# Kernel optimization log

Measured on AMD Instinct MI355X. Metric: run time of the kernel, lower is better.

## Reference

```python
import jax, jax.numpy as jnp
import numpy as np

NE, NU, E = 200000, 100000, 1000000
F_IN, H, OUT = 64, 128, 2
GRID_SIZE, K = 5, 3  # efficient-kan defaults: grid_size=5, spline_order=3
NB = GRID_SIZE + K    # number of b-spline bases per input feature = 8


def make_grid(in_features):
    h = 2.0 / GRID_SIZE  # grid_range [-1, 1]
    g = jnp.arange(-K, GRID_SIZE + K + 1, dtype=jnp.float32) * h - 1.0  # [GRID_SIZE+2K+1]
    return jnp.tile(g[None, :], (in_features, 1))  # [in, 12]


def b_splines(x, grid):
    # x: [N, in], grid: [in, G]; Cox-de Boor recursion -> [N, in, G-K-1]
    x = x[..., None]
    bases = ((x >= grid[:, :-1]) & (x < grid[:, 1:])).astype(x.dtype)
    for j in range(1, K + 1):
        bases = ((x - grid[:, :-(j + 1)]) / (grid[:, j:-1] - grid[:, :-(j + 1)])) * bases[..., :-1] \
              + ((grid[:, j + 1:] - x) / (grid[:, j + 1:] - grid[:, 1:-j])) * bases[..., 1:]
    return bases


def kan_linear(x, base_w, spline_w, scaler, grid):
    base = jax.nn.silu(x) @ base_w.T                       # [N, out]
    sw = spline_w * scaler[..., None]                      # [out, in, NB]
    spline = jnp.einsum('nik,oik->no', b_splines(x, grid), sw)
    return base + spline


def sage_conv(x_src, x_dst, ei, w_n, b_n, w_r):
    # PyG SAGEConv: lin_l(mean_j x_j) + lin_r(x_i); bias only on lin_l
    src, dst = ei[0], ei[1]
    msg = jnp.take(x_src, src, axis=0)                                  # [E, H] gather
    s = jax.ops.segment_sum(msg, dst, num_segments=x_dst.shape[0])      # scatter-sum
    cnt = jax.ops.segment_sum(jnp.ones(src.shape, x_src.dtype), dst, num_segments=x_dst.shape[0])
    mean = s / jnp.maximum(cnt, 1.0)[:, None]
    return mean @ w_n.T + b_n + x_dst @ w_r.T


def setup_inputs():
    key = jax.random.key(0)
    ks = jax.random.split(key, 40)
    inp = {}
    inp['x_email'] = jax.random.normal(ks[0], (NE, F_IN), jnp.float32)
    inp['ei_ue'] = jnp.stack([jax.random.randint(ks[1], (E,), 0, NU),
                              jax.random.randint(ks[2], (E,), 0, NE)])
    inp['ei_eu'] = jnp.stack([jax.random.randint(ks[3], (E,), 0, NE),
                              jax.random.randint(ks[4], (E,), 0, NU)])
    inp['w_email'] = jax.random.normal(ks[5], (H, F_IN), jnp.float32) * 0.05
    inp['b_email'] = jnp.zeros((H,), jnp.float32)
    inp['emb_user'] = jax.random.normal(ks[6], (NU, H), jnp.float32) * 0.05
    i = 7
    for name in ['l1_ue', 'l1_eu', 'l2_ue', 'l2_eu']:
        inp['w_' + name + '_n'] = jax.random.normal(ks[i], (H, H), jnp.float32) * 0.05; i += 1
        inp['b_' + name] = jnp.zeros((H,), jnp.float32)
        inp['w_' + name + '_r'] = jax.random.normal(ks[i], (H, H), jnp.float32) * 0.05; i += 1
    inp['kan1_base'] = jax.random.normal(ks[i], (64, H), jnp.float32) * 0.05; i += 1
    inp['kan1_spline'] = jax.random.normal(ks[i], (64, H, NB), jnp.float32) * 0.05; i += 1
    inp['kan1_scaler'] = 1.0 + jax.random.normal(ks[i], (64, H), jnp.float32) * 0.05; i += 1
    inp['grid1'] = make_grid(H)
    inp['kan2_base'] = jax.random.normal(ks[i], (OUT, 64), jnp.float32) * 0.05; i += 1
    inp['kan2_spline'] = jax.random.normal(ks[i], (OUT, 64, NB), jnp.float32) * 0.05; i += 1
    inp['kan2_scaler'] = 1.0 + jax.random.normal(ks[i], (OUT, 64), jnp.float32) * 0.05; i += 1
    inp['grid2'] = make_grid(64)
    return inp


def reference(x_email, ei_ue, ei_eu, w_email, b_email, emb_user,
              w_l1_ue_n, b_l1_ue, w_l1_ue_r, w_l1_eu_n, b_l1_eu, w_l1_eu_r,
              w_l2_ue_n, b_l2_ue, w_l2_ue_r, w_l2_eu_n, b_l2_eu, w_l2_eu_r,
              kan1_base, kan1_spline, kan1_scaler, grid1,
              kan2_base, kan2_spline, kan2_scaler, grid2):
    xe = x_email @ w_email.T + b_email      # email_lin
    xu = emb_user                            # embedding(arange(NU)) == full table
    # hetero SAGE layer 1 (to_hetero aggr='sum'; one inbound edge type per dst)
    e1 = jax.nn.relu(sage_conv(xu, xe, ei_ue, w_l1_ue_n, b_l1_ue, w_l1_ue_r))
    u1 = jax.nn.relu(sage_conv(xe, xu, ei_eu, w_l1_eu_n, b_l1_eu, w_l1_eu_r))
    # dropout(p=0.5) is identity in eval mode
    # layer 2: only the email output feeds the KAN head (user-dst conv2 output is unused)
    e2 = jax.nn.relu(sage_conv(u1, e1, ei_ue, w_l2_ue_n, b_l2_ue, w_l2_ue_r))
    h = kan_linear(e2, kan1_base, kan1_spline, kan1_scaler, grid1)
    out = kan_linear(h, kan2_base, kan2_spline, kan2_scaler, grid2)
    return out
```

## Files before the change

### kernel.cpp

```cpp
#include <hip/hip_runtime.h>
#include <hip/hip_bf16.h>

typedef __attribute__((ext_vector_type(8))) short short8;
typedef __attribute__((ext_vector_type(4))) float f32x4;

static constexpr int kNE  = 200000;
static constexpr int kNU  = 100000;
static constexpr int kE   = 1000000;
static constexpr int kGrpU = kNE / 8;
static constexpr int kGrpE = kNU / 8;

static constexpr long long SZ_NEH = (long long)kNE * 128;
static constexpr long long SZ_NUH = (long long)kNU * 128;
static constexpr long long O_B0   = 64;
static constexpr long long O_B1   = O_B0 + SZ_NEH;
static constexpr long long O_B2   = O_B1 + SZ_NEH;
static constexpr long long O_W    = O_B2 + SZ_NUH;
static constexpr long long O_BEM  = O_W;
static constexpr long long O_BL1  = O_BEM + 128;
static constexpr long long O_BEN  = O_BL1 + 128;
static constexpr long long O_BL2  = O_BEN + 128;
static constexpr long long O_GRID1= O_BL2 + 128;
static constexpr long long O_BASE2= O_GRID1 + 1536;
static constexpr long long O_GRID2= O_BASE2 + 128;
static constexpr long long O_SW2  = O_GRID2 + 768;
static constexpr long long I_CNT_UE = O_SW2 + 1024;
static constexpr long long I_CNT_EU = I_CNT_UE + kNE;
static constexpr long long I_RO_UE  = I_CNT_EU + kNU;
static constexpr long long I_RO_EU  = I_RO_UE + kNE;
static constexpr long long I_CUR_UE = I_RO_EU + kNU;
static constexpr long long I_CUR_EU = I_CUR_UE + kNE;
static constexpr long long I_SRT_UE = I_CUR_EU + kNU;
static constexpr long long I_SRT_EU = I_SRT_UE + kE;
static constexpr long long I_BSUM_UE= I_SRT_EU + kE;
static constexpr long long I_BOFF_UE= I_BSUM_UE + 256;
static constexpr long long I_BSUM_EU= I_BOFF_UE + 256;
static constexpr long long I_BOFF_EU= I_BSUM_EU + 256;
static constexpr long long FR_BASE_I= (I_BOFF_EU + 256 + 7) & ~7LL;
static constexpr long long U_WEM   = 0;
static constexpr long long U_W1N   = U_WEM + 8192;
static constexpr long long U_W1R   = U_W1N + 16384;
static constexpr long long U_WEN   = U_W1R + 16384;
static constexpr long long U_WER   = U_WEN + 16384;
static constexpr long long U_W2N   = U_WER + 16384;
static constexpr long long U_W2R   = U_W2N + 16384;
static constexpr long long U_BASE1 = U_W2R + 16384;
static constexpr long long U_SW1H  = U_BASE1 + 8192;
static constexpr long long U_SW1L  = U_SW1H + 65536;

__device__ __forceinline__ float bf2f(unsigned short u) {
    return __uint_as_float(((unsigned)u) << 16);
}
__device__ __forceinline__ unsigned short f2bf_rne(float f) {
    unsigned u = __float_as_uint(f);
    return (unsigned short)((u + 0x7fffu + ((u >> 16) & 1u)) >> 16);
}
__device__ __forceinline__ void split2(float x, unsigned short& hi, unsigned short& lo) {
    hi = f2bf_rne(x);
    lo = f2bf_rne(x - bf2f(hi));
}
__device__ __forceinline__ float btrunc(float x) {
    return __uint_as_float(__float_as_uint(x) & 0xffff0000u);
}
__device__ __forceinline__ unsigned pack_hi2(float x0, float x1) {
    return __builtin_amdgcn_perm(__float_as_uint(x1), __float_as_uint(x0), 0x07060302u);
}
__device__ __forceinline__ void split8_trunc(const float* __restrict__ xv, short8& ah, short8& al) {
    unsigned* hp = (unsigned*)&ah;
    unsigned* lp = (unsigned*)&al;
#pragma unroll
    for (int jp = 0; jp < 4; jp++) {
        const float x0 = xv[2 * jp], x1 = xv[2 * jp + 1];
        const float l0 = x0 - btrunc(x0), l1 = x1 - btrunc(x1);
        hp[jp] = pack_hi2(x0, x1);
        lp[jp] = pack_hi2(l0, l1);
    }
}
__device__ __forceinline__ int get_isbf(const unsigned* __restrict__ g) {
    return (g[0] == 0xC00CCCCDu) ? 0 : 1;
}

__device__ __forceinline__ void pack128_one(const void* __restrict__ src, unsigned short* __restrict__ dst,
                                            int K, int t, int isbf) {
    const int lane = t & 63;
    const int nt = (t >> 6) % 8;
    const int kt = (t >> 6) / 8;
    const int n = nt * 16 + (lane & 15);
    const int k0 = kt * 32 + (lane >> 4) * 8;
    unsigned short* d = dst + (((size_t)(kt * 8 + nt) * 64 + lane) << 3);
#pragma unroll
    for (int j = 0; j < 8; j++) {
        float f = isbf ? bf2f(((const unsigned short*)src)[(size_t)n * K + k0 + j])
                       : ((const float*)src)[(size_t)n * K + k0 + j];
        d[j] = f2bf_rne(f);
    }
}

__device__ __forceinline__ void base1_one(const void* __restrict__ src, unsigned short* __restrict__ dst,
                                          int t, int isbf) {
    const int lane = t & 63, nt = (t >> 6) & 3, kt = t >> 8;
    const int n = nt * 16 + (lane & 15);
    const int k0 = kt * 32 + (lane >> 4) * 8;
    unsigned short* d = dst + (((size_t)(kt * 4 + nt) * 64 + lane) << 3);
#pragma unroll
    for (int j = 0; j < 8; j++) {
        float f = isbf ? bf2f(((const unsigned short*)src)[n * 128 + k0 + j])
                       : ((const float*)src)[n * 128 + k0 + j];
        d[j] = f2bf_rne(f);
    }
}

__device__ __forceinline__ void sw1_one(const void* __restrict__ sp, const void* __restrict__ sc,
                                        unsigned short* __restrict__ dh, unsigned short* __restrict__ dl,
                                        int t, int isbf) {
    const int lane = t & 63, nt = (t >> 6) & 3, kt = t >> 8;
    const int n = nt * 16 + (lane & 15);
    const int k0 = kt * 32 + (lane >> 4) * 8;
    const float scal = isbf ? bf2f(((const unsigned short*)sc)[n * 128 + (k0 >> 3)])
                            : ((const float*)sc)[n * 128 + (k0 >> 3)];
    const size_t base = ((size_t)(kt * 4 + nt) * 64 + lane) << 3;
#pragma unroll
    for (int j = 0; j < 8; j++) {
        float f = isbf ? bf2f(((const unsigned short*)sp)[(size_t)n * 1024 + k0 + j])
                       : ((const float*)sp)[(size_t)n * 1024 + k0 + j];
        float p = f * scal;
        unsigned short hi, lo;
        split2(p, hi, lo);
        dh[base + j] = hi;
        dl[base + j] = lo;
    }
}

struct PrepArgs {
    const void* csrc[7];  int coff[7];  int cn[7];
    const void* psrc[7];  unsigned pdst[7];  int pK[7];
    const void* sp2;  const void* sc2;
    const void* b1src;  const void* swsp;  const void* swsc;
};

__global__ __launch_bounds__(256) void prep_kernel(PrepArgs A, float* __restrict__ wsf,
                                                   int* __restrict__ wsi,
                                                   unsigned short* __restrict__ fbase,
                                                   const unsigned* __restrict__ gdet) {
    const int isbf = get_isbf(gdet);
    const int t0 = blockIdx.x * 256 + threadIdx.x;
    const int gs = gridDim.x * 256;
    for (int i = t0; i < kNE + kNU; i += gs) wsi[I_CNT_UE + i] = 0;
    for (int t = 0; t < 7; t++) {
        const int n = A.cn[t];
        const void* s = A.csrc[t];
        float* d = wsf + A.coff[t];
        for (int i = t0; i < n; i += gs)
            d[i] = isbf ? bf2f(((const unsigned short*)s)[i]) : ((const float*)s)[i];
    }
    for (int i = t0; i < 1024; i += gs) {
        float a = isbf ? bf2f(((const unsigned short*)A.sp2)[i]) : ((const float*)A.sp2)[i];
        float b = isbf ? bf2f(((const unsigned short*)A.sc2)[i >> 3]) : ((const float*)A.sc2)[i >> 3];
        wsf[O_SW2 + i] = a * b;
    }
    for (int t = 0; t < 7; t++) {
        const int K = A.pK[t];
        const int tot = (K / 32) * 8 * 64;
        unsigned short* dst = fbase + A.pdst[t];
        const void* src = A.psrc[t];
        for (int i = t0; i < tot; i += gs) pack128_one(src, dst, K, i, isbf);
    }
    for (int i = t0; i < 1024; i += gs) base1_one(A.b1src, fbase + U_BASE1, i, isbf);
    for (int i = t0; i < 8192; i += gs)
        sw1_one(A.swsp, A.swsc, fbase + U_SW1H, fbase + U_SW1L, i, isbf);
}

__global__ __launch_bounds__(256) void hist_both(const int* __restrict__ ue, const int* __restrict__ eu,
                                                 int* __restrict__ cntU, int* __restrict__ cntE) {
    const int g = blockIdx.x & 7;
    const int loU = g * kGrpU, hiU = loU + kGrpU;
    const int loE = g * kGrpE, hiE = loE + kGrpE;
    const int stride = (gridDim.x >> 3) * 256;
    for (int i = (blockIdx.x >> 3) * 256 + threadIdx.x; i < kE; i += stride) {
        const int d = ue[kE + i];
        if (d >= loU && d < hiU) atomicAdd(&cntU[d], 1);
        const int d2 = eu[kE + i];
        if (d2 >= loE && d2 < hiE) atomicAdd(&cntE[d2], 1);
    }
}

__global__ __launch_bounds__(256) void scan1_both(const int* __restrict__ cntU, int* __restrict__ roU,
                                                  int* __restrict__ bsU, const int* __restrict__ cntE,
                                                  int* __restrict__ roE, int* __restrict__ bsE) {
    __shared__ int sc[256];
    int b = blockIdx.x;
    const int* cnt;  int* ro;  int* bsum;  int n;
    if (b < 196) { cnt = cntU; ro = roU; bsum = bsU; n = kNE; }
    else { b -= 196; cnt = cntE; ro = roE; bsum = bsE; n = kNU; }
    const int t = threadIdx.x;
    const int i0 = b * 1024 + t * 4;
    int c[4];
#pragma unroll
    for (int q = 0; q < 4; q++) c[q] = (i0 + q < n) ? cnt[i0 + q] : 0;
    int s = c[0] + c[1] + c[2] + c[3];
    sc[t] = s;
    __syncthreads();
    for (int off = 1; off < 256; off <<= 1) {
        int v = (t >= off) ? sc[t - off] : 0;
        __syncthreads();
        sc[t] += v;
        __syncthreads();
    }
    int run = sc[t] - s;
#pragma unroll
    for (int q = 0; q < 4; q++) {
        if (i0 + q < n) ro[i0 + q] = run;
        run += c[q];
    }
    if (t == 255) bsum[b] = sc[255];
}

__global__ __launch_bounds__(256) void scan2_both(const int* __restrict__ bsU, int* __restrict__ boU,
                                                  const int* __restrict__ bsE, int* __restrict__ boE) {
    __shared__ int sc[256];
    const int* bsum;  int* boff;  int nb;
    if (blockIdx.x == 0) { bsum = bsU; boff = boU; nb = 196; }
    else { bsum = bsE; boff = boE; nb = 98; }
    const int t = threadIdx.x;
    int s = (t < nb) ? bsum[t] : 0;
    sc[t] = s;
    __syncthreads();
    for (int off = 1; off < 256; off <<= 1) {
        int v = (t >= off) ? sc[t - off] : 0;
        __syncthreads();
        sc[t] += v;
        __syncthreads();
    }
    if (t < nb) boff[t] = sc[t] - s;
}

__global__ __launch_bounds__(256) void scan3_both(int* __restrict__ roU, int* __restrict__ curU,
                                                  const int* __restrict__ boU, int* __restrict__ roE,
                                                  int* __restrict__ curE, const int* __restrict__ boE) {
    const int stride = gridDim.x * blockDim.x;
    for (int i = blockIdx.x * blockDim.x + threadIdx.x; i < kNE + kNU; i += stride) {
        if (i < kNE) {
            int v = roU[i] + boU[i >> 10];
            roU[i] = v;
            curU[i] = v;
        } else {
            int j = i - kNE;
            int v = roE[j] + boE[j >> 10];
            roE[j] = v;
            curE[j] = v;
        }
    }
}

__global__ __launch_bounds__(256) void fill_both(const int* __restrict__ ue, const int* __restrict__ eu,
                                                 int* __restrict__ curU, int* __restrict__ srtU,
                                                 int* __restrict__ curE, int* __restrict__ srtE) {
    const int g = blockIdx.x & 7;
    const int loU = g * kGrpU, hiU = loU + kGrpU;
    const int loE = g * kGrpE, hiE = loE + kGrpE;
    const int stride = (gridDim.x >> 3) * 256;
    for (int i = (blockIdx.x >> 3) * 256 + threadIdx.x; i < kE; i += stride) {
        const int d = ue[kE + i];
        if (d >= loU && d < hiU) {
            const int pos = atomicAdd(&curU[d], 1);
            srtU[pos] = ue[i];
        }
        const int d2 = eu[kE + i];
        if (d2 >= loE && d2 < hiE) {
            const int pos = atomicAdd(&curE[d2], 1);
            srtE[pos] = eu[i];
        }
    }
}

template <int KD, bool RAW, int THREADS>
__device__ __forceinline__ void stage_tile(float (*Xs)[132], const void* __restrict__ Av, int r0, int N,
                                           int tid, int isbf) {
    constexpr int TPR = THREADS / 64;
    constexpr int per = KD / TPR;
    const int row = tid / TPR;
    const int cq = (tid % TPR) * per;
    const size_t gr = (size_t)min(r0 + row, N - 1);
    if (RAW && isbf) {
        const unsigned short* p = (const unsigned short*)Av + gr * KD + cq;
#pragma unroll
        for (int v = 0; v < per; v += 8) {
            short8 s = *(const short8*)(p + v);
#pragma unroll
            for (int j = 0; j < 8; j++) Xs[row][cq + v + j] = bf2f(((unsigned short*)&s)[j]);
        }
    } else {
        const float* p = (const float*)Av + gr * KD + cq;
#pragma unroll
        for (int v = 0; v < per; v += 4) *(float4*)&Xs[row][cq + v] = *(const float4*)(p + v);
    }
}

template <int KT, int NT>
__device__ __forceinline__ void gemm_phase(float (*Xs)[132], const unsigned short* __restrict__ Wf,
                                           f32x4* acc, int rowl, int q, int lane, int ntBase) {
#pragma unroll
    for (int kt = 0; kt < KT; kt++) {
        float xv[8];
        *(float4*)&xv[0] = *(const float4*)&Xs[rowl][kt * 32 + q * 8];
        *(float4*)&xv[4] = *(const float4*)&Xs[rowl][kt * 32 + q * 8 + 4];
        short8 ah, al;
        split8_trunc(xv, ah, al);
#pragma unroll
        for (int nt = 0; nt < NT; nt++) {
            short8 b = *(const short8*)(Wf + (((size_t)(kt * 8 + ntBase + nt) * 64 + lane) << 3));
            acc[nt] = __builtin_amdgcn_mfma_f32_16x16x32_bf16(ah, b, acc[nt], 0, 0, 0);
            acc[nt] = __builtin_amdgcn_mfma_f32_16x16x32_bf16(al, b, acc[nt], 0, 0, 0);
        }
    }
}

__global__ __launch_bounds__(256) void lin_xe(const void* __restrict__ A1,
                                              const unsigned short* __restrict__ W1f,
                                              const float* __restrict__ bias, float* __restrict__ out, int N,
                                              const unsigned* __restrict__ gdet) {
    __shared__ float Xs[64][132];
    const int tid = threadIdx.x;
    const int wave = tid >> 6, lane = tid & 63;
    const int m = lane & 15, q = lane >> 4;
    const int r0 = blockIdx.x * 64;
    const int isbf = get_isbf(gdet);
    const int rowl = wave * 16 + m;
    f32x4 acc[8] = {};

    stage_tile<64, true, 256>(Xs, A1, r0, N, tid, isbf);
    __syncthreads();
    gemm_phase<2, 8>(Xs, W1f, acc, rowl, q, lane, 0);

    float bv[8];
#pragma unroll
    for (int nt = 0; nt < 8; nt++) bv[nt] = bias[nt * 16 + m];
#pragma unroll
    for (int r = 0; r < 4; r++) {
        int grow = r0 + wave * 16 + q * 4 + r;
        if (grow < N) {
#pragma unroll
            for (int nt = 0; nt < 8; nt++)
                out[(size_t)grow * 128 + nt * 16 + m] = acc[nt][r] + bv[nt];
        }
    }
}

template <bool RAWG>
__device__ __forceinline__ float2 gload(const void* __restrict__ G, int s, int lane, int isbf) {
    if (RAWG && isbf) {
        const ushort2 v = *(const ushort2*)((const unsigned short*)G + (size_t)s * 128 + lane * 2);
        return make_float2(bf2f(v.x), bf2f(v.y));
    }
    return *(const float2*)((const float*)G + (size_t)s * 128 + lane * 2);
}

template <bool RAWG, bool RAW2>
__global__ __launch_bounds__(512, 8) void agglin_mfma(const void* __restrict__ Gsrc, const void* __restrict__ A2,
                                                   const unsigned short* __restrict__ W1f,
                                                   const unsigned short* __restrict__ W2f,
                                                   const float* __restrict__ bias, float* __restrict__ out,
                                                   const int* __restrict__ ro, const int* __restrict__ cnt,
                                                   const int* __restrict__ sorted, int N,
                                                   const unsigned* __restrict__ gdet) {
    __shared__ float Xs[64][132];
    const int tid = threadIdx.x;
    const int wave = tid >> 6, lane = tid & 63;
    const int m = lane & 15, q = lane >> 4;
    const int wg = wave >> 1;
    const int wh = wave & 1;
    const int r0 = blockIdx.x * 64;
    const int isbf = get_isbf(gdet);

    int beg8[8], cnt8[8];
#pragma unroll
    for (int rr = 0; rr < 8; rr++) {
        const int n = r0 + wave * 8 + rr;
        beg8[rr] = (n < N) ? ro[n] : 0;
        cnt8[rr] = (n < N) ? cnt[n] : 0;
    }

#pragma unroll 1
    for (int rr = 0; rr < 8; rr++) {
        const int lrow = wave * 8 + rr;
        const int beg = beg8[rr];
        const int end = beg + cnt8[rr];
        float ax = 0.f, ay = 0.f;
        float a1x = 0.f, a1y = 0.f, a2x = 0.f, a2y = 0.f, a3x = 0.f, a3y = 0.f;
        int p = beg;
        for (; p + 3 < end; p += 4) {
            const int s0 = sorted[p], s1 = sorted[p + 1], s2 = sorted[p + 2], s3 = sorted[p + 3];
            const float2 v0 = gload<RAWG>(Gsrc, s0, lane, isbf);
            const float2 v1 = gload<RAWG>(Gsrc, s1, lane, isbf);
            const float2 v2 = gload<RAWG>(Gsrc, s2, lane, isbf);
            const float2 v3 = gload<RAWG>(Gsrc, s3, lane, isbf);
            ax += v0.x;  ay += v0.y;
            a1x += v1.x; a1y += v1.y;
            a2x += v2.x; a2y += v2.y;
            a3x += v3.x; a3y += v3.y;
        }
        for (; p < end; p++) {
            const float2 v = gload<RAWG>(Gsrc, sorted[p], lane, isbf);
            ax += v.x;
            ay += v.y;
        }
        ax += a1x + a2x + a3x;
        ay += a1y + a2y + a3y;
        const int deg = end - beg;
        const float inv = (deg > 0) ? 1.f / (float)deg : 0.f;
        Xs[lrow][lane * 2] = ax * inv;
        Xs[lrow][lane * 2 + 1] = ay * inv;
    }
    __syncthreads();

    const int rowl = wg * 16 + m;
    const int ntBase = wh * 4;
    f32x4 acc[4] = {};

    gemm_phase<4, 4>(Xs, W1f, acc, rowl, q, lane, ntBase);

    __syncthreads();
    stage_tile<128, RAW2, 512>(Xs, A2, r0, N, tid, isbf);
    __syncthreads();
    gemm_phase<4, 4>(Xs, W2f, acc, rowl, q, lane, ntBase);

    float bv[4];
#pragma unroll
    for (int nt = 0; nt < 4; nt++) bv[nt] = bias[(ntBase + nt) * 16 + m];
#pragma unroll
    for (int r = 0; r < 4; r++) {
        int grow = r0 + wg * 16 + q * 4 + r;
        if (grow < N) {
#pragma unroll
            for (int nt = 0; nt < 4; nt++) {
                float v = acc[nt][r] + bv[nt];
                out[(size_t)grow * 128 + (ntBase + nt) * 16 + m] = fmaxf(v, 0.f);
            }
        }
    }
}

__device__ __forceinline__ void bases8u(float x, float t0, float invh, float* __restrict__ b) {
    const float sp = (x - t0) * invh;
    const float fi = floorf(sp);
    const float u = sp - fi;
    const int i = (int)fi;
    const float u2 = u * u, u3 = u2 * u;
    const float v = 1.f - u;
    const float p0 = u3 * (1.f / 6.f);
    const float p1 = fmaf(-0.5f, u3, fmaf(0.5f, u2, fmaf(0.5f, u, 1.f / 6.f)));
    const float p2 = fmaf(0.5f, u3, fmaf(-1.f, u2, 2.f / 3.f));
    const float p3 = v * v * v * (1.f / 6.f);
#pragma unroll
    for (int j = 0; j < 8; j++) {
        float r = (i == j) ? p0 : 0.f;
        r = (i == j + 1) ? p1 : r;
        r = (i == j + 2) ? p2 : r;
        r = (i == j + 3) ? p3 : r;
        b[j] = r;
    }
}

__device__ __forceinline__ void bases8u_frag(float x, float t0, float invh, short8& bh, short8& bl) {
    const float sp = (x - t0) * invh;
    const float fi = floorf(sp);
    const float u = sp - fi;
    int i = (int)fi;
    i = max(-1, min(11, i));
    const float u2 = u * u, u3 = u2 * u;
    const float v = 1.f - u;
    const float p0 = u3 * (1.f / 6.f);
    const float p1 = fmaf(-0.5f, u3, fmaf(0.5f, u2, fmaf(0.5f, u, 1.f / 6.f)));
    const float p2 = fmaf(0.5f, u3, fmaf(-1.f, u2, 2.f / 3.f));
    const float p3 = v * (v * v) * (1.f / 6.f);
    const float q0 = p0 - btrunc(p0), q1 = p1 - btrunc(p1);
    const float q2 = p2 - btrunc(p2), q3 = p3 - btrunc(p3);
    const unsigned long long Ph = (((unsigned long long)pack_hi2(p1, p0)) << 32) | pack_hi2(p3, p2);
    const unsigned long long Pl = (((unsigned long long)pack_hi2(q1, q0)) << 32) | pack_hi2(q3, q2);
    const int t = 16 * i - 48;
    const unsigned sa = (unsigned)t & 63u;
    const unsigned sb = (unsigned)(-t) & 63u;
    const unsigned sc = (unsigned)(64 - t) & 63u;
    const unsigned sd = (unsigned)(t - 64) & 63u;
    const bool neg = t < 0;
    const bool ok0 = t >= -48;
    const bool lt64 = t < 64;
    const bool gt0 = t > 0;
    const bool lt128 = t < 128;
    const unsigned long long h0 = neg ? (ok0 ? (Ph >> sb) : 0ull) : (lt64 ? (Ph << sa) : 0ull);
    const unsigned long long h1 = neg ? 0ull : (lt64 ? (gt0 ? (Ph >> sc) : 0ull)
                                                     : (lt128 ? (Ph << sd) : 0ull));
    const unsigned long long g0 = neg ? (ok0 ? (Pl >> sb) : 0ull) : (lt64 ? (Pl << sa) : 0ull);
    const unsigned long long g1 = neg ? 0ull : (lt64 ? (gt0 ? (Pl >> sc) : 0ull)
                                                     : (lt128 ? (Pl << sd) : 0ull));
    unsigned long long* bhp = (unsigned long long*)&bh;
    unsigned long long* blp = (unsigned long long*)&bl;
    bhp[0] = h0; bhp[1] = h1;
    blp[0] = g0; blp[1] = g1;
}

__global__ __launch_bounds__(256) void kan1_mfma(const float* __restrict__ X,
                                                 const unsigned short* __restrict__ basef,
                                                 const unsigned short* __restrict__ swh,
                                                 const unsigned short* __restrict__ swl,
                                                 const float* __restrict__ grid, float* __restrict__ Hout) {
    __shared__ float Xs[64][128];
    const int tid = threadIdx.x;
    const int wave = tid >> 6, lane = tid & 63;
    const int m = lane & 15, q = lane >> 4;
    const int r0 = blockIdx.x * 64;

    const float t0 = grid[0];
    const float invh = 1.f / (grid[1] - grid[0]);

    {
        const int row = tid >> 2, cq = (tid & 3) * 32;
        const int sw = (row & 7) << 2;
        const float* p = &X[(size_t)(r0 + row) * 128 + cq];
#pragma unroll
        for (int v = 0; v < 8; v++) *(float4*)&Xs[row][(cq + v * 4) ^ sw] = *(const float4*)(p + v * 4);
    }
    __syncthreads();

    const int rowl = wave * 16 + m;
    const int swr = (rowl & 7) << 2;
    f32x4 acc[4] = {};

#pragma unroll
    for (int kt = 0; kt < 4; kt++) {
        float xv[8];
        *(float4*)&xv[0] = *(const float4*)&Xs[rowl][(kt * 32 + q * 8) ^ swr];
        *(float4*)&xv[4] = *(const float4*)&Xs[rowl][(kt * 32 + q * 8 + 4) ^ swr];
        float sv[8];
#pragma unroll
        for (int j = 0; j < 8; j++) {
            float x = xv[j];
            sv[j] = x / (1.f + __expf(-x));
        }
        short8 ah, al;
        split8_trunc(sv, ah, al);
#pragma unroll
        for (int nt = 0; nt < 4; nt++) {
            short8 b = *(const short8*)(basef + (((size_t)(kt * 4 + nt) * 64 + lane) << 3));
            acc[nt] = __builtin_amdgcn_mfma_f32_16x16x32_bf16(ah, b, acc[nt], 0, 0, 0);
            acc[nt] = __builtin_amdgcn_mfma_f32_16x16x32_bf16(al, b, acc[nt], 0, 0, 0);
        }
    }

    const unsigned short* __restrict__ whp = swh + ((size_t)lane << 3);
    const unsigned short* __restrict__ wlp = swl + ((size_t)lane << 3);
    short8 wAh[4], wAl[4], wBh[4], wBl[4];
#pragma unroll
    for (int nt = 0; nt < 4; nt++) {
        wAh[nt] = *(const short8*)(whp + nt * 512);
        wAl[nt] = *(const short8*)(wlp + nt * 512);
    }
    float xE = Xs[rowl][q ^ swr];
#pragma unroll 1
    for (int kt2 = 0; kt2 < 16; kt2++) {
        const int ko = 2 * kt2 + 1;
#pragma unroll
        for (int nt = 0; nt < 4; nt++) {
            wBh[nt] = *(const short8*)(whp + ko * 2048 + nt * 512);
            wBl[nt] = *(const short8*)(wlp + ko * 2048 + nt * 512);
        }
        const float xO = Xs[rowl][(ko * 4 + q) ^ swr];
        {
            short8 bh, bl;
            bases8u_frag(xE, t0, invh, bh, bl);
#pragma unroll
            for (int nt = 0; nt < 4; nt++) {
                acc[nt] = __builtin_amdgcn_mfma_f32_16x16x32_bf16(bh, wAh[nt], acc[nt], 0, 0, 0);
                acc[nt] = __builtin_amdgcn_mfma_f32_16x16x32_bf16(bl, wAh[nt], acc[nt], 0, 0, 0);
                acc[nt] = __builtin_amdgcn_mfma_f32_16x16x32_bf16(bh, wAl[nt], acc[nt], 0, 0, 0);
            }
        }
        if (kt2 < 15) {
            const int ke2 = 2 * kt2 + 2;
#pragma unroll
            for (int nt = 0; nt < 4; nt++) {
                wAh[nt] = *(const short8*)(whp + ke2 * 2048 + nt * 512);
                wAl[nt] = *(const short8*)(wlp + ke2 * 2048 + nt * 512);
            }
            xE = Xs[rowl][(ke2 * 4 + q) ^ swr];
        }
        {
            short8 bh, bl;
            bases8u_frag(xO, t0, invh, bh, bl);
#pragma unroll
            for (int nt = 0; nt < 4; nt++) {
                acc[nt] = __builtin_amdgcn_mfma_f32_16x16x32_bf16(bh, wBh[nt], acc[nt], 0, 0, 0);
                acc[nt] = __builtin_amdgcn_mfma_f32_16x16x32_bf16(bl, wBh[nt], acc[nt], 0, 0, 0);
                acc[nt] = __builtin_amdgcn_mfma_f32_16x16x32_bf16(bh, wBl[nt], acc[nt], 0, 0, 0);
            }
        }
    }

#pragma unroll
    for (int r = 0; r < 4; r++) {
        int grow = r0 + wave * 16 + q * 4 + r;
#pragma unroll
        for (int nt = 0; nt < 4; nt++) Hout[(size_t)grow * 64 + nt * 16 + m] = acc[nt][r];
    }
}

__global__ __launch_bounds__(256) void kan2_kernel(const float* __restrict__ h, const float* __restrict__ base2,
                                                   const float* __restrict__ sw2, const float* __restrict__ grid2,
                                                   void* __restrict__ out, const unsigned* __restrict__ gdet) {
    const int lane = threadIdx.x & 63;
    const int wid = (blockIdx.x * blockDim.x + threadIdx.x) >> 6;
    const int nw = (gridDim.x * blockDim.x) >> 6;
    const int k = lane;
    const float t0 = grid2[0];
    const float invh = 1.f / (grid2[1] - grid2[0]);
    const float wb0 = base2[k], wb1 = base2[64 + k];
    float ws0[8], ws1[8];
#pragma unroll
    for (int j = 0; j < 8; j++) { ws0[j] = sw2[k * 8 + j]; ws1[j] = sw2[512 + k * 8 + j]; }
    const int isbf = get_isbf(gdet);

    for (int n = wid; n < kNE; n += nw) {
        float x = h[(size_t)n * 64 + k];
        float sil = x / (1.f + __expf(-x));
        float b[8];
        bases8u(x, t0, invh, b);
        float o0 = sil * wb0, o1 = sil * wb1;
#pragma unroll
        for (int j = 0; j < 8; j++) {
            o0 = fmaf(b[j], ws0[j], o0);
            o1 = fmaf(b[j], ws1[j], o1);
        }
#pragma unroll
        for (int off = 32; off > 0; off >>= 1) {
            o0 += __shfl_down(o0, off, 64);
            o1 += __shfl_down(o1, off, 64);
        }
        if (lane == 0) {
            if (isbf) {
                __hip_bfloat16* ob = (__hip_bfloat16*)out;
                ob[(size_t)n * 2] = __float2bfloat16(o0);
                ob[(size_t)n * 2 + 1] = __float2bfloat16(o1);
            } else {
                ((float2*)out)[n] = make_float2(o0, o1);
            }
        }
    }
}

extern "C" void kernel_launch(void* const* d_in, const int* in_sizes, int n_in, void* d_out, int out_size,
                              void* d_ws, size_t ws_size, hipStream_t stream) {
    (void)in_sizes; (void)n_in; (void)out_size; (void)ws_size;
    float* wsf = (float*)d_ws;
    int* wsi = (int*)d_ws;
    unsigned short* fbase = (unsigned short*)(wsi + FR_BASE_I);
    const unsigned* gdet = (const unsigned*)d_in[21];

    PrepArgs A;
    const int csrc[7] = {4, 7, 10, 13, 21, 22, 25};
    const long long coff[7] = {O_BEM, O_BL1, O_BEN, O_BL2, O_GRID1, O_BASE2, O_GRID2};
    const int cn[7] = {128, 128, 128, 128, 1536, 128, 768};
    for (int t = 0; t < 7; t++) {
        A.csrc[t] = d_in[csrc[t]];
        A.coff[t] = (int)coff[t];
        A.cn[t] = cn[t];
    }
    const int psrc[7] = {3, 6, 8, 9, 11, 12, 14};
    const long long pdst[7] = {U_WEM, U_W1N, U_W1R, U_WEN, U_WER, U_W2N, U_W2R};
    const int pK[7] = {64, 128, 128, 128, 128, 128, 128};
    for (int t = 0; t < 7; t++) {
        A.psrc[t] = d_in[psrc[t]];
        A.pdst[t] = (unsigned)pdst[t];
        A.pK[t] = pK[t];
    }
    A.sp2 = d_in[23];
    A.sc2 = d_in[24];
    A.b1src = d_in[18];
    A.swsp = d_in[19];
    A.swsc = d_in[20];
    prep_kernel<<<512, 256, 0, stream>>>(A, wsf, wsi, fbase, gdet);

    const int* ei_ue = (const int*)d_in[1];
    const int* ei_eu = (const int*)d_in[2];

    hist_both<<<2048, 256, 0, stream>>>(ei_ue, ei_eu, wsi + I_CNT_UE, wsi + I_CNT_EU);
    scan1_both<<<294, 256, 0, stream>>>(wsi + I_CNT_UE, wsi + I_RO_UE, wsi + I_BSUM_UE,
                                        wsi + I_CNT_EU, wsi + I_RO_EU, wsi + I_BSUM_EU);
    scan2_both<<<2, 256, 0, stream>>>(wsi + I_BSUM_UE, wsi + I_BOFF_UE, wsi + I_BSUM_EU, wsi + I_BOFF_EU);
    scan3_both<<<512, 256, 0, stream>>>(wsi + I_RO_UE, wsi + I_CUR_UE, wsi + I_BOFF_UE,
                                        wsi + I_RO_EU, wsi + I_CUR_EU, wsi + I_BOFF_EU);
    fill_both<<<2048, 256, 0, stream>>>(ei_ue, ei_eu, wsi + I_CUR_UE, wsi + I_SRT_UE,
                                        wsi + I_CUR_EU, wsi + I_SRT_EU);

    lin_xe<<<3125, 256, 0, stream>>>(d_in[0], fbase + U_WEM, wsf + O_BEM, wsf + O_B0, kNE, gdet);

    agglin_mfma<true, false><<<3125, 512, 0, stream>>>(
        d_in[5], wsf + O_B0, fbase + U_W1N, fbase + U_W1R, wsf + O_BL1, wsf + O_B1,
        wsi + I_RO_UE, wsi + I_CNT_UE, wsi + I_SRT_UE, kNE, gdet);

    agglin_mfma<false, true><<<1563, 512, 0, stream>>>(
        wsf + O_B0, d_in[5], fbase + U_WEN, fbase + U_WER, wsf + O_BEN, wsf + O_B2,
        wsi + I_RO_EU, wsi + I_CNT_EU, wsi + I_SRT_EU, kNU, gdet);

    agglin_mfma<false, false><<<3125, 512, 0, stream>>>(
        wsf + O_B2, wsf + O_B1, fbase + U_W2N, fbase + U_W2R, wsf + O_BL2, wsf + O_B0,
        wsi + I_RO_UE, wsi + I_CNT_UE, wsi + I_SRT_UE, kNE, gdet);

    kan1_mfma<<<3125, 256, 0, stream>>>(wsf + O_B0, fbase + U_BASE1, fbase + U_SW1H, fbase + U_SW1L,
                                        wsf + O_GRID1, wsf + O_B1);
    kan2_kernel<<<2048, 256, 0, stream>>>(wsf + O_B1, wsf + O_BASE2, wsf + O_SW2, wsf + O_GRID2, d_out, gdet);
}
```

Before: 923.8 us.

## Split KAN1 reduction dimension across wave pairs with LDS partial-sum reduction

After: 1.630 ms. +76.4%, slower.

```diff
diff --git a/kernel.cpp b/kernel.cpp
--- a/kernel.cpp
+++ b/kernel.cpp
@@ -499,7 +499,7 @@
     blp[0] = g0; blp[1] = g1;
 }
 
-__global__ __launch_bounds__(256) void kan1_mfma(const float* __restrict__ X,
+__global__ __launch_bounds__(512, 8) void kan1_mfma(const float* __restrict__ X,
                                                  const unsigned short* __restrict__ basef,
                                                  const unsigned short* __restrict__ swh,
                                                  const unsigned short* __restrict__ swl,
@@ -508,26 +508,29 @@
     const int tid = threadIdx.x;
     const int wave = tid >> 6, lane = tid & 63;
     const int m = lane & 15, q = lane >> 4;
+    const int wg2 = wave >> 1;
+    const int kh = wave & 1;
     const int r0 = blockIdx.x * 64;
 
     const float t0 = grid[0];
     const float invh = 1.f / (grid[1] - grid[0]);
 
     {
-        const int row = tid >> 2, cq = (tid & 3) * 32;
+        const int row = tid >> 3, cq = (tid & 7) * 16;
         const int sw = (row & 7) << 2;
         const float* p = &X[(size_t)(r0 + row) * 128 + cq];
 #pragma unroll
-        for (int v = 0; v < 8; v++) *(float4*)&Xs[row][(cq + v * 4) ^ sw] = *(const float4*)(p + v * 4);
-    }
-    __syncthreads();
-
-    const int rowl = wave * 16 + m;
+        for (int v = 0; v < 4; v++) *(float4*)&Xs[row][(cq + v * 4) ^ sw] = *(const float4*)(p + v * 4);
+    }
+    __syncthreads();
+
+    const int rowl = wg2 * 16 + m;
     const int swr = (rowl & 7) << 2;
     f32x4 acc[4] = {};
 
 #pragma unroll
-    for (int kt = 0; kt < 4; kt++) {
+    for (int kk = 0; kk < 2; kk++) {
+        const int kt = kh * 2 + kk;
         float xv[8];
         *(float4*)&xv[0] = *(const float4*)&Xs[rowl][(kt * 32 + q * 8) ^ swr];
         *(float4*)&xv[4] = *(const float4*)&Xs[rowl][(kt * 32 + q * 8 + 4) ^ swr];
@@ -547,24 +550,25 @@
         }
     }
 
-    const unsigned short* __restrict__ whp = swh + ((size_t)lane << 3);
-    const unsigned short* __restrict__ wlp = swl + ((size_t)lane << 3);
+    const int ktBase = kh * 16;
+    const unsigned short* __restrict__ whp = swh + ((size_t)ktBase * 2048) + ((size_t)lane << 3);
+    const unsigned short* __restrict__ wlp = swl + ((size_t)ktBase * 2048) + ((size_t)lane << 3);
     short8 wAh[4], wAl[4], wBh[4], wBl[4];
 #pragma unroll
     for (int nt = 0; nt < 4; nt++) {
         wAh[nt] = *(const short8*)(whp + nt * 512);
         wAl[nt] = *(const short8*)(wlp + nt * 512);
     }
-    float xE = Xs[rowl][q ^ swr];
+    float xE = Xs[rowl][(ktBase * 4 + q) ^ swr];
 #pragma unroll 1
-    for (int kt2 = 0; kt2 < 16; kt2++) {
+    for (int kt2 = 0; kt2 < 8; kt2++) {
         const int ko = 2 * kt2 + 1;
 #pragma unroll
         for (int nt = 0; nt < 4; nt++) {
             wBh[nt] = *(const short8*)(whp + ko * 2048 + nt * 512);
             wBl[nt] = *(const short8*)(wlp + ko * 2048 + nt * 512);
         }
-        const float xO = Xs[rowl][(ko * 4 + q) ^ swr];
+        const float xO = Xs[rowl][((ktBase + ko) * 4 + q) ^ swr];
         {
             short8 bh, bl;
             bases8u_frag(xE, t0, invh, bh, bl);
@@ -575,14 +579,14 @@
                 acc[nt] = __builtin_amdgcn_mfma_f32_16x16x32_bf16(bh, wAl[nt], acc[nt], 0, 0, 0);
             }
         }
-        if (kt2 < 15) {
+        if (kt2 < 7) {
             const int ke2 = 2 * kt2 + 2;
 #pragma unroll
             for (int nt = 0; nt < 4; nt++) {
                 wAh[nt] = *(const short8*)(whp + ke2 * 2048 + nt * 512);
                 wAl[nt] = *(const short8*)(wlp + ke2 * 2048 + nt * 512);
             }
-            xE = Xs[rowl][(ke2 * 4 + q) ^ swr];
+            xE = Xs[rowl][((ktBase + ke2) * 4 + q) ^ swr];
         }
         {
             short8 bh, bl;
@@ -596,11 +600,26 @@
         }
     }
 
-#pragma unroll
-    for (int r = 0; r < 4; r++) {
-        int grow = r0 + wave * 16 + q * 4 + r;
-#pragma unroll
-        for (int nt = 0; nt < 4; nt++) Hout[(size_t)grow * 64 + nt * 16 + m] = acc[nt][r];
+    __syncthreads();
+    float* red = &Xs[0][0];
+    const int rb = (wg2 * 64 + lane) * 20;
+    if (kh == 1) {
+#pragma unroll
+        for (int nt = 0; nt < 4; nt++) *(f32x4*)&red[rb + nt * 4] = acc[nt];
+    }
+    __syncthreads();
+    if (kh == 0) {
+#pragma unroll
+        for (int nt = 0; nt < 4; nt++) {
+            const f32x4 pv = *(const f32x4*)&red[rb + nt * 4];
+            acc[nt] += pv;
+        }
+#pragma unroll
+        for (int r = 0; r < 4; r++) {
+            int grow = r0 + wg2 * 16 + q * 4 + r;
+#pragma unroll
+            for (int nt = 0; nt < 4; nt++) Hout[(size_t)grow * 64 + nt * 16 + m] = acc[nt][r];
+        }
     }
 }
 
@@ -705,7 +724,7 @@
         wsf + O_B2, wsf + O_B1, fbase + U_W2N, fbase + U_W2R, wsf + O_BL2, wsf + O_B0,
         wsi + I_RO_UE, wsi + I_CNT_UE, wsi + I_SRT_UE, kNE, gdet);
 
-    kan1_mfma<<<3125, 256, 0, stream>>>(wsf + O_B0, fbase + U_BASE1, fbase + U_SW1H, fbase + U_SW1L,
+    kan1_mfma<<<3125, 512, 0, stream>>>(wsf + O_B0, fbase + U_BASE1, fbase + U_SW1H, fbase + U_SW1L,
                                         wsf + O_GRID1, wsf + O_B1);
     kan2_kernel<<<2048, 256, 0, stream>>>(wsf + O_B1, wsf + O_BASE2, wsf + O_SW2, wsf + O_GRID2, d_out, gdet);
 }
```
